# Kernel optimization log

Hardware: AMD Instinct MI355X
Metric: run time of the kernel (lower is better)

The kernel has to match this reference:

```python
import jax, jax.numpy as jnp
import numpy as np

N, D, F, C = 50000, 16, 128, 40  # nodes, fixed neighbor count, feat dim (hidden/2), classes


def _w(k, shape, fan_in):
    return jax.random.normal(k, shape, jnp.float32) / np.float32(np.sqrt(fan_in))


def setup_inputs() -> dict:
    key = jax.random.key(0)
    ks = jax.random.split(key, 8)
    z = lambda *s: jnp.zeros(s, jnp.float32)
    inp = {
        "x": jax.random.normal(ks[0], (N, F), jnp.float32),
        "edge_src": jax.random.randint(ks[1], (N, D), 0, N),  # dst is implicitly arange(N), sorted
        "W1": _w(ks[2], (F, F), F), "b1": z(F),
        "W2": _w(ks[3], (3 * F, F), F), "b2": z(3 * F),
        "W3": _w(ks[4], (F, 3 * F), 3 * F), "b3": z(F),
    }
    for i, (kb, oc) in (("1", (ks[5], F)), ("2", (ks[6], C))):
        pass  # placeholder (loop built below)
    for i, kb, oc in (("1", ks[5], F), ("2", ks[6], C)):
        kk = jax.random.split(kb, 5)
        inp["Wp" + i] = _w(kk[0], (F, F), F); inp["bp" + i] = z(F)
        inp["Wih" + i] = _w(kk[1], (4 * F, F), F)
        inp["Whh" + i] = _w(kk[2], (4 * F, F), F)
        inp["bih" + i] = z(4 * F); inp["bhh" + i] = z(4 * F)
        inp["Wl" + i] = _w(kk[3], (oc, F), F); inp["bl" + i] = z(oc)
        inp["Wr" + i] = _w(kk[4], (oc, F), F)
    return inp


def lstm_last(seq, Wih, Whh, bih, bhh):
    """seq: [N, T, F] -> final hidden state [N, H] (torch LSTM gate order i,f,g,o)."""
    Hh = Whh.shape[1]
    b = bih + bhh

    def step(carry, xt):
        h, c = carry
        g = xt @ Wih.T + h @ Whh.T + b
        i, f, gg, o = jnp.split(g, 4, axis=-1)
        c = jax.nn.sigmoid(f) * c + jax.nn.sigmoid(i) * jnp.tanh(gg)
        h = jax.nn.sigmoid(o) * jnp.tanh(c)
        return (h, c), None

    h0 = jnp.zeros((seq.shape[0], Hh), seq.dtype)
    (h, _), _ = jax.lax.scan(step, (h0, h0), jnp.swapaxes(seq, 0, 1))
    return h


def sage_conv_lstm(x, edge_src, Wp, bp, Wih, Whh, bih, bhh, Wl, bl, Wr):
    """PyG SAGEConv(aggr='lstm', project=True) with fixed per-node degree D."""
    xp = jax.nn.relu(x @ Wp.T + bp)           # project source features
    msgs = xp[edge_src]                        # [N, D, F] neighbor gather (sorted by dst)
    aggr = lstm_last(msgs, Wih, Whh, bih, bhh)  # LSTM over each neighborhood
    return aggr @ Wl.T + bl + x @ Wr.T         # lin_l(aggr) + lin_r(root)


def reference(x, edge_src, W1, b1, W2, b2, W3, b3,
              Wp1, bp1, Wih1, Whh1, bih1, bhh1, Wl1, bl1, Wr1,
              Wp2, bp2, Wih2, Whh2, bih2, bhh2, Wl2, bl2, Wr2):
    # Dead MLP branch: original forward computes it then overwrites h with conv1(x, ...)
    h = jax.nn.relu(x @ W1.T + b1)
    h = jax.nn.relu(h @ W2.T + b2)
    h = jax.nn.relu(h @ W3.T + b3)
    del h
    h = jax.nn.relu(sage_conv_lstm(x, edge_src, Wp1, bp1, Wih1, Whh1, bih1, bhh1, Wl1, bl1, Wr1))
    return sage_conv_lstm(h, edge_src, Wp2, bp2, Wih2, Whh2, bih2, bhh2, Wl2, bl2, Wr2)
```

## Files before the change

### kernel.cpp

```cpp
#include <hip/hip_runtime.h>
#include <hip/hip_bf16.h>


typedef __hip_bfloat16 bf16;
typedef __attribute__((ext_vector_type(8))) short short8;
typedef __attribute__((ext_vector_type(4))) short short4v;
typedef __attribute__((ext_vector_type(4))) float floatx4;

#define LOG2E 1.4426950408889634f
#define TWOL  2.8853900817779268f

__device__ __forceinline__ float bf2f(bf16 v) { return __bfloat162float(v); }
__device__ __forceinline__ bf16  f2bf(float v) { return __float2bfloat16(v); }
__device__ __forceinline__ float bfs2f(short s) {
    union { float f; unsigned u; } v; v.u = ((unsigned)(unsigned short)s) << 16; return v.f;
}
__device__ __forceinline__ short f2bfs(float v) {
    bf16 b = __float2bfloat16(v); return *(short*)&b;
}

__device__ __forceinline__ float ex2(float x) {
#if __has_builtin(__builtin_amdgcn_exp2f)
    return __builtin_amdgcn_exp2f(x);
#else
    return exp2f(x);
#endif
}

__device__ __forceinline__ float cell(float i_, float f_, float g_, float o_, float& c) {
    float ei = ex2(-i_), ef = ex2(-f_), eg = ex2(g_), eo = ex2(-o_);
    float A = (1.f + ei) * (eg + 1.f);
    float B = 1.f + ef;
    float cn = fmaf(c, A, fmaf(eg, TWOL, -TWOL) * B) * __builtin_amdgcn_rcpf(A * B);
    c = cn;
    float ec = ex2(cn);
    return (ec - 1.f) * __builtin_amdgcn_rcpf((ec + 1.f) * (1.f + eo));
}

__device__ __forceinline__ int ydecode(int p) {
    int pw = (p >> 6) & 7, pq = (p >> 4) & 3, pg = (p >> 2) & 3, pr = p & 3;
    return pg * 128 + pw * 16 + pq * 4 + pr;
}

__device__ __forceinline__ void dma2(const bf16* gp, void* lp0, void* lp1) {
    __builtin_amdgcn_global_load_lds(
        (const __attribute__((address_space(1))) void*)gp,
        (__attribute__((address_space(3))) void*)lp0, 16, 0, 0);
    __builtin_amdgcn_global_load_lds(
        (const __attribute__((address_space(1))) void*)(gp + 32),
        (__attribute__((address_space(3))) void*)lp1, 16, 0, 0);
}

struct Cvt { const void* src; bf16* dst; int n; int gs; };
struct CvtAll { Cvt t[19]; };

typedef __attribute__((ext_vector_type(4))) float float4v;

__global__ void convert_inputs(CvtAll ca, int* __restrict__ flag) {
    __shared__ int sflag;
    {
        const unsigned short* xb = (const unsigned short*)ca.t[0].src;
        int cnt = 0;
        for (int i = threadIdx.x; i < 1024; i += blockDim.x) {
            int e = (xb[i] >> 7) & 0xFF;
            cnt += (e >= 0xC8);
        }
        if (threadIdx.x == 0) sflag = 0;
        __syncthreads();
        if (cnt) atomicAdd(&sflag, cnt);
        __syncthreads();
    }
    const bool isf32 = (sflag >= 16);
    if (blockIdx.x == 0 && threadIdx.x == 0) *flag = isf32 ? 1 : 0;

    const int stride = gridDim.x * blockDim.x;
    const int tid0 = blockIdx.x * blockDim.x + threadIdx.x;
#pragma unroll 1
    for (int k = 0; k < 19; k++) {
        const int n = ca.t[k].n, gs = ca.t[k].gs;
        const int n8 = n >> 3;
        bf16* d = ca.t[k].dst;
        for (int i = tid0; i < n8; i += stride) {
            const int base = i << 3;
            float m = 1.f;
            if (gs) m = ((((unsigned)base >> gs) & 3) == 2) ? TWOL : LOG2E;
            short8 ov;
            if (isf32) {
                const float4v* sp = (const float4v*)ca.t[k].src;
                float4v a = sp[2 * i], b = sp[2 * i + 1];
#pragma unroll
                for (int j = 0; j < 4; j++) {
                    ov[j]     = f2bfs(a[j] * m);
                    ov[4 + j] = f2bfs(b[j] * m);
                }
            } else {
                short8 sv = ((const short8*)ca.t[k].src)[i];
                if (gs) {
#pragma unroll
                    for (int j = 0; j < 8; j++) ov[j] = f2bfs(bfs2f(sv[j]) * m);
                } else ov = sv;
            }
            ((short8*)d)[i] = ov;
        }
        for (int i = (n8 << 3) + tid0; i < n; i += stride) {
            float v = isf32 ? ((const float*)ca.t[k].src)[i]
                            : bfs2f(((const short*)ca.t[k].src)[i]);
            if (gs) v *= ((((unsigned)i >> gs) & 3) == 2) ? TWOL : LOG2E;
            d[i] = f2bf(v);
        }
    }
}

template <int NCT, bool RELU, bool BIAS2, bool DUAL, bool OUTF>
__global__ __launch_bounds__(256, 2) void gemm_bias(
    const bf16* __restrict__ A, const bf16* __restrict__ B,
    const bf16* __restrict__ bias, const bf16* __restrict__ bias2,
    const bf16* __restrict__ A2, const bf16* __restrict__ B2,
    void* __restrict__ Cv, const int* __restrict__ oflag,
    int N, int nbt, int ldc)
{
    const int tid = threadIdx.x;
    const int w = tid >> 6, l = tid & 63, q = l >> 4, lid = l & 15;
    const int rowbase = blockIdx.x * 64 + w * 16;
    const int colslice = blockIdx.y * (NCT * 16);

    int arow = rowbase + lid;
    if (arow >= N) arow = N - 1;

    floatx4 acc[NCT];
#pragma unroll
    for (int ct = 0; ct < NCT; ct++) acc[ct] = (floatx4)(0.f);

    short8 bfrag[NCT][4];
#pragma unroll
    for (int ct = 0; ct < NCT; ct++) {
        int j = colslice + ct * 16 + lid;
        if (j >= nbt) j = nbt - 1;
#pragma unroll
        for (int kt = 0; kt < 4; kt++)
            bfrag[ct][kt] = *(const short8*)(B + (size_t)j * 128 + kt * 32 + q * 8);
    }
#pragma unroll
    for (int kt = 0; kt < 4; kt++) {
        short8 af = *(const short8*)(A + (size_t)arow * 128 + kt * 32 + q * 8);
#pragma unroll
        for (int ct = 0; ct < NCT; ct++)
            acc[ct] = __builtin_amdgcn_mfma_f32_16x16x32_bf16(af, bfrag[ct][kt], acc[ct], 0, 0, 0);
    }
    if constexpr (DUAL) {
#pragma unroll
        for (int ct = 0; ct < NCT; ct++) {
            int j = colslice + ct * 16 + lid;
            if (j >= nbt) j = nbt - 1;
#pragma unroll
            for (int kt = 0; kt < 4; kt++)
                bfrag[ct][kt] = *(const short8*)(B2 + (size_t)j * 128 + kt * 32 + q * 8);
        }
#pragma unroll
        for (int kt = 0; kt < 4; kt++) {
            short8 af = *(const short8*)(A2 + (size_t)arow * 128 + kt * 32 + q * 8);
#pragma unroll
            for (int ct = 0; ct < NCT; ct++)
                acc[ct] = __builtin_amdgcn_mfma_f32_16x16x32_bf16(af, bfrag[ct][kt], acc[ct], 0, 0, 0);
        }
    }
    bool of32 = false;
    if constexpr (OUTF) of32 = (*oflag != 0);
#pragma unroll
    for (int ct = 0; ct < NCT; ct++) {
        int cg = colslice + ct * 16 + lid;
        int cb = cg < nbt ? cg : nbt - 1;
        float bv = bf2f(bias[cb]);
        if constexpr (BIAS2) bv += bf2f(bias2[cb]);
#pragma unroll
        for (int r = 0; r < 4; r++) {
            int row = rowbase + q * 4 + r;
            float v = acc[ct][r] + bv;
            if constexpr (RELU) v = fmaxf(v, 0.f);
            if (row < N && cg < nbt) {
                size_t idx = (size_t)row * ldc + cg;
                if constexpr (OUTF) {
                    if (of32) ((float*)Cv)[idx] = v;
                    else      ((bf16*)Cv)[idx] = f2bf(v);
                } else {
                    ((bf16*)Cv)[idx] = f2bf(v);
                }
            }
        }
    }
}

__global__ __launch_bounds__(256, 2) void fused_xp_y(
    const bf16* __restrict__ X, const bf16* __restrict__ Wp, const bf16* __restrict__ bp,
    const bf16* __restrict__ Wih, const bf16* __restrict__ bih, const bf16* __restrict__ bhh,
    bf16* __restrict__ Yout, int N)
{
    __shared__ bf16 T[64][136];
    const int tid = threadIdx.x;
    const int w = tid >> 6, l = tid & 63, q = l >> 4, lid = l & 15;
    const int rowbase = blockIdx.x * 64;

    int arow = rowbase + w * 16 + lid;
    if (arow >= N) arow = N - 1;

    floatx4 acc[8];
    short8 bfrag[8][4];
    float bvv[8];

#pragma unroll
    for (int ct = 0; ct < 8; ct++) acc[ct] = (floatx4)(0.f);
#pragma unroll
    for (int ct = 0; ct < 8; ct++) {
        int j = lid * 8 + ct;
        bvv[ct] = bf2f(bp[j]);
#pragma unroll
        for (int kt = 0; kt < 4; kt++)
            bfrag[ct][kt] = *(const short8*)(Wp + (size_t)j * 128 + kt * 32 + q * 8);
    }
#pragma unroll
    for (int kt = 0; kt < 4; kt++) {
        short8 af = *(const short8*)(X + (size_t)arow * 128 + kt * 32 + q * 8);
#pragma unroll
        for (int ct = 0; ct < 8; ct++)
            acc[ct] = __builtin_amdgcn_mfma_f32_16x16x32_bf16(af, bfrag[ct][kt], acc[ct], 0, 0, 0);
    }
#pragma unroll
    for (int r = 0; r < 4; r++) {
        short8 ov;
#pragma unroll
        for (int ct = 0; ct < 8; ct++)
            ov[ct] = f2bfs(fmaxf(acc[ct][r] + bvv[ct], 0.f));
        *(short8*)&T[w * 16 + q * 4 + r][lid * 8] = ov;
    }
    __syncthreads();

#pragma unroll 1
    for (int cc = 0; cc < 4; cc++) {
#pragma unroll
        for (int ct = 0; ct < 8; ct++) {
            int src = ydecode(cc * 128 + lid * 8 + ct);
            bvv[ct] = bf2f(bih[src]) + bf2f(bhh[src]);
#pragma unroll
            for (int kt = 0; kt < 4; kt++)
                bfrag[ct][kt] = *(const short8*)(Wih + (size_t)src * 128 + kt * 32 + q * 8);
        }
#pragma unroll
        for (int ct = 0; ct < 8; ct++) acc[ct] = (floatx4)(0.f);
#pragma unroll
        for (int kt = 0; kt < 4; kt++) {
            short8 af = *(const short8*)&T[w * 16 + lid][kt * 32 + q * 8];
#pragma unroll
            for (int ct = 0; ct < 8; ct++)
                acc[ct] = __builtin_amdgcn_mfma_f32_16x16x32_bf16(af, bfrag[ct][kt], acc[ct], 0, 0, 0);
        }
#pragma unroll
        for (int r = 0; r < 4; r++) {
            int row = rowbase + w * 16 + q * 4 + r;
            if (row < N) {
                short8 ov;
#pragma unroll
                for (int ct = 0; ct < 8; ct++)
                    ov[ct] = f2bfs(acc[ct][r] + bvv[ct]);
                *(short8*)(Yout + (size_t)row * 512 + cc * 128 + lid * 8) = ov;
            }
        }
    }
}

__global__ __launch_bounds__(256, 2) void fused_lin_xp_y(
    const bf16* __restrict__ aggr, const bf16* __restrict__ Wl, const bf16* __restrict__ bl,
    const bf16* __restrict__ X, const bf16* __restrict__ Wr,
    bf16* __restrict__ h1out,
    const bf16* __restrict__ Wp2, const bf16* __restrict__ bp2,
    const bf16* __restrict__ Wih2, const bf16* __restrict__ bih2, const bf16* __restrict__ bhh2,
    bf16* __restrict__ Yout, int N)
{
    __shared__ bf16 T1[64][136];
    __shared__ bf16 T2[64][136];
    const int tid = threadIdx.x;
    const int w = tid >> 6, l = tid & 63, q = l >> 4, lid = l & 15;
    const int rowbase = blockIdx.x * 64;

    int arow = rowbase + w * 16 + lid;
    if (arow >= N) arow = N - 1;

    floatx4 acc[8];
    short8 bfrag[8][4];
    float bvv[8];

#pragma unroll
    for (int ct = 0; ct < 8; ct++) acc[ct] = (floatx4)(0.f);
#pragma unroll
    for (int ct = 0; ct < 8; ct++) {
        int j = lid * 8 + ct;
        bvv[ct] = bf2f(bl[j]);
#pragma unroll
        for (int kt = 0; kt < 4; kt++)
            bfrag[ct][kt] = *(const short8*)(Wl + (size_t)j * 128 + kt * 32 + q * 8);
    }
#pragma unroll
    for (int kt = 0; kt < 4; kt++) {
        short8 af = *(const short8*)(aggr + (size_t)arow * 128 + kt * 32 + q * 8);
#pragma unroll
        for (int ct = 0; ct < 8; ct++)
            acc[ct] = __builtin_amdgcn_mfma_f32_16x16x32_bf16(af, bfrag[ct][kt], acc[ct], 0, 0, 0);
    }
#pragma unroll
    for (int ct = 0; ct < 8; ct++) {
        int j = lid * 8 + ct;
#pragma unroll
        for (int kt = 0; kt < 4; kt++)
            bfrag[ct][kt] = *(const short8*)(Wr + (size_t)j * 128 + kt * 32 + q * 8);
    }
#pragma unroll
    for (int kt = 0; kt < 4; kt++) {
        short8 af = *(const short8*)(X + (size_t)arow * 128 + kt * 32 + q * 8);
#pragma unroll
        for (int ct = 0; ct < 8; ct++)
            acc[ct] = __builtin_amdgcn_mfma_f32_16x16x32_bf16(af, bfrag[ct][kt], acc[ct], 0, 0, 0);
    }
#pragma unroll
    for (int r = 0; r < 4; r++) {
        short8 ov;
#pragma unroll
        for (int ct = 0; ct < 8; ct++)
            ov[ct] = f2bfs(fmaxf(acc[ct][r] + bvv[ct], 0.f));
        int rl = w * 16 + q * 4 + r;
        *(short8*)&T1[rl][lid * 8] = ov;
        int row = rowbase + rl;
        if (row < N) *(short8*)(h1out + (size_t)row * 128 + lid * 8) = ov;
    }
    __syncthreads();

#pragma unroll
    for (int ct = 0; ct < 8; ct++) {
        int j = lid * 8 + ct;
        bvv[ct] = bf2f(bp2[j]);
#pragma unroll
        for (int kt = 0; kt < 4; kt++)
            bfrag[ct][kt] = *(const short8*)(Wp2 + (size_t)j * 128 + kt * 32 + q * 8);
    }
#pragma unroll
    for (int ct = 0; ct < 8; ct++) acc[ct] = (floatx4)(0.f);
#pragma unroll
    for (int kt = 0; kt < 4; kt++) {
        short8 af = *(const short8*)&T1[w * 16 + lid][kt * 32 + q * 8];
#pragma unroll
        for (int ct = 0; ct < 8; ct++)
            acc[ct] = __builtin_amdgcn_mfma_f32_16x16x32_bf16(af, bfrag[ct][kt], acc[ct], 0, 0, 0);
    }
#pragma unroll
    for (int r = 0; r < 4; r++) {
        short8 ov;
#pragma unroll
        for (int ct = 0; ct < 8; ct++)
            ov[ct] = f2bfs(fmaxf(acc[ct][r] + bvv[ct], 0.f));
        *(short8*)&T2[w * 16 + q * 4 + r][lid * 8] = ov;
    }
    __syncthreads();

#pragma unroll 1
    for (int cc = 0; cc < 4; cc++) {
#pragma unroll
        for (int ct = 0; ct < 8; ct++) {
            int src = ydecode(cc * 128 + lid * 8 + ct);
            bvv[ct] = bf2f(bih2[src]) + bf2f(bhh2[src]);
#pragma unroll
            for (int kt = 0; kt < 4; kt++)
                bfrag[ct][kt] = *(const short8*)(Wih2 + (size_t)src * 128 + kt * 32 + q * 8);
        }
#pragma unroll
        for (int ct = 0; ct < 8; ct++) acc[ct] = (floatx4)(0.f);
#pragma unroll
        for (int kt = 0; kt < 4; kt++) {
            short8 af = *(const short8*)&T2[w * 16 + lid][kt * 32 + q * 8];
#pragma unroll
            for (int ct = 0; ct < 8; ct++)
                acc[ct] = __builtin_amdgcn_mfma_f32_16x16x32_bf16(af, bfrag[ct][kt], acc[ct], 0, 0, 0);
        }
#pragma unroll
        for (int r = 0; r < 4; r++) {
            int row = rowbase + w * 16 + q * 4 + r;
            if (row < N) {
                short8 ov;
#pragma unroll
                for (int ct = 0; ct < 8; ct++)
                    ov[ct] = f2bfs(acc[ct][r] + bvv[ct]);
                *(short8*)(Yout + (size_t)row * 512 + cc * 128 + lid * 8) = ov;
            }
        }
    }
}

__global__ __launch_bounds__(512, 4) void lstm_aggr(
    const bf16* __restrict__ Y,
    const int* __restrict__ esrc,
    const bf16* __restrict__ Whh,
    bf16* __restrict__ aggr,
    int N)
{
    __shared__ alignas(16) short stage[2][8][1024];
    __shared__ alignas(16) bf16 hb[2][16][136];
    __shared__ int srcl[16][16];

    const int tid = threadIdx.x;
    const int w = tid >> 6, l = tid & 63, q = l >> 4, lid = l & 15;
    const int nodebase = blockIdx.x * 16;

    if (tid < 256) {
        int node = tid >> 4, t = tid & 15;
        srcl[t][node] = esrc[(size_t)(nodebase + node) * 16 + t];
    }

    short8 wf[4][4];
#pragma unroll
    for (int g = 0; g < 4; g++) {
        int gc = g * 128 + 16 * w + lid;
#pragma unroll
        for (int kt = 0; kt < 4; kt++)
            wf[g][kt] = *(const short8*)(Whh + (size_t)gc * 128 + kt * 32 + q * 8);
    }

    float c[4];
#pragma unroll
    for (int r = 0; r < 4; r++) c[r] = 0.f;

    const int laneoff = w * 64 + q * 8;

    __syncthreads();

    {
        int s0 = srcl[0][lid];
        dma2(Y + (size_t)s0 * 512 + laneoff, &stage[0][w][0], &stage[0][w][512]);
        int s1 = srcl[1][lid];
        dma2(Y + (size_t)s1 * 512 + laneoff, &stage[1][w][0], &stage[1][w][512]);
    }

#pragma unroll 2
    for (int t = 0; t < 16; t++) {
        const int cb = t & 1;

        if (t == 15) asm volatile("s_waitcnt vmcnt(0)" ::: "memory");
        else         asm volatile("s_waitcnt vmcnt(2)" ::: "memory");

        int snext = (t < 14) ? srcl[t + 2][lid] : 0;

        floatx4 acc[4];
        {
            const short* wbuf = &stage[cb][w][0];
            short8 y0 = *(const short8*)&wbuf[q * 256 + lid * 8];
            short8 y1 = *(const short8*)&wbuf[q * 256 + 128 + lid * 8];
#pragma unroll
            for (int g = 0; g < 2; g++)
#pragma unroll
                for (int r = 0; r < 4; r++) {
                    acc[g][r]     = bfs2f(y0[g * 4 + r]);
                    acc[2 + g][r] = bfs2f(y1[g * 4 + r]);
                }
        }

        if (t) {
#pragma unroll
            for (int kt = 0; kt < 4; kt++) {
                short8 bh = *(const short8*)&hb[cb][lid][kt * 32 + q * 8];
#pragma unroll
                for (int g = 0; g < 4; g++)
                    acc[g] = __builtin_amdgcn_mfma_f32_16x16x32_bf16(wf[g][kt], bh, acc[g], 0, 0, 0);
            }
        }

        {
            short4v hv;
#pragma unroll
            for (int r = 0; r < 4; r++)
                hv[r] = f2bfs(cell(acc[0][r], acc[1][r], acc[2][r], acc[3][r], c[r]));
            if (t < 15) *(short4v*)&hb[cb ^ 1][lid][16 * w + 4 * q] = hv;
            else        *(short4v*)(aggr + (size_t)(nodebase + lid) * 128 + 16 * w + 4 * q) = hv;
        }

        if (t < 15) {
            asm volatile("s_waitcnt lgkmcnt(0)" ::: "memory");
            if (t < 14)
                dma2(Y + (size_t)snext * 512 + laneoff, &stage[cb][w][0], &stage[cb][w][512]);
            __builtin_amdgcn_s_barrier();
        }
    }
}

extern "C" void kernel_launch(void* const* d_in, const int* in_sizes, int n_in,
                              void* d_out, int out_size, void* d_ws, size_t ws_size,
                              hipStream_t stream)
{
    const int N = 50000;
    const int* es = (const int*)d_in[1];
    char* ws = (char*)d_ws;

    static const int idxs[19] = {0, 8,9,10,11,12,13,14,15,16, 17,18,19,20,21,22,23,24,25};
    static const int gss[19]  = {0, 0,0,14,14,7,7,0,0,0, 0,0,14,14,7,7,0,0,0};
    bf16* conv[19];
    size_t off = 0;
    CvtAll ca;
    for (int k = 0; k < 19; k++) {
        conv[k] = (bf16*)ws + off;
        ca.t[k].src = d_in[idxs[k]];
        ca.t[k].dst = conv[k];
        ca.t[k].n = in_sizes[idxs[k]];
        ca.t[k].gs = gss[k];
        off += (size_t)((in_sizes[idxs[k]] + 63) & ~63);
    }
    int* flag = (int*)(ws + ((size_t)15 << 20));
    bf16* aggr = (bf16*)(ws + ((size_t)16 << 20));
    bf16* Y    = (bf16*)(ws + ((size_t)30 << 20));
    bf16* h1   = (bf16*)(ws + ((size_t)84 << 20));

    const bf16 *xc  = conv[0];
    const bf16 *Wp1 = conv[1],  *bp1 = conv[2],  *Wih1 = conv[3],  *Whh1 = conv[4];
    const bf16 *bih1 = conv[5], *bhh1 = conv[6], *Wl1 = conv[7],   *bl1 = conv[8],  *Wr1 = conv[9];
    const bf16 *Wp2 = conv[10], *bp2 = conv[11], *Wih2 = conv[12], *Whh2 = conv[13];
    const bf16 *bih2 = conv[14], *bhh2 = conv[15], *Wl2 = conv[16], *bl2 = conv[17], *Wr2 = conv[18];

    dim3 blk(256);
    const int gx = (N + 63) / 64;
    const int gl = N / 16;

    convert_inputs<<<dim3(1024), blk, 0, stream>>>(ca, flag);

    fused_xp_y<<<dim3(gx), blk, 0, stream>>>(xc, Wp1, bp1, Wih1, bih1, bhh1, Y, N);
    lstm_aggr<<<dim3(gl), dim3(512), 0, stream>>>(Y, es, Whh1, aggr, N);

    fused_lin_xp_y<<<dim3(gx), blk, 0, stream>>>(
        aggr, Wl1, bl1, xc, Wr1, h1, Wp2, bp2, Wih2, bih2, bhh2, Y, N);
    lstm_aggr<<<dim3(gl), dim3(512), 0, stream>>>(Y, es, Whh2, aggr, N);

    gemm_bias<3, false, false, true, true><<<dim3(gx, 1), blk, 0, stream>>>(
        aggr, Wl2, bl2, nullptr, h1, Wr2, d_out, flag, N, 40, 40);
}
```

Measured before the change: 670.7 us.

## Fuse final linear layer into second LSTM kernel and pre-permute Wih weights

The final output GEMM (lin_l of aggr plus lin_r of h1) moves into the epilogue of the second LSTM aggregation kernel. The last hidden state stays in LDS and goes straight into MFMA, so one kernel launch and the aggr write/read round trip are gone. The conversion kernel also pre-permutes Wih rows into the ydecode order and precomputes the fp32 bias sum, which removes the index decode and double bias loads in the projection kernels. The cost is extra epilogue work and register pressure in the LSTM kernel, where only 3 of 8 waves do the tail GEMM.

```diff
diff --git a/kernel.cpp b/kernel.cpp
--- a/kernel.cpp
+++ b/kernel.cpp
@@ -6,6 +6,7 @@
 typedef __attribute__((ext_vector_type(8))) short short8;
 typedef __attribute__((ext_vector_type(4))) short short4v;
 typedef __attribute__((ext_vector_type(4))) float floatx4;
+typedef __attribute__((ext_vector_type(4))) float float4v;
 
 #define LOG2E 1.4426950408889634f
 #define TWOL  2.8853900817779268f
@@ -51,10 +52,8 @@
         (__attribute__((address_space(3))) void*)lp1, 16, 0, 0);
 }
 
-struct Cvt { const void* src; bf16* dst; int n; int gs; };
-struct CvtAll { Cvt t[19]; };
-
-typedef __attribute__((ext_vector_type(4))) float float4v;
+struct Cvt { const void* src; const void* src2; bf16* dst; int n; int mode; };
+struct CvtAll { Cvt t[17]; };
 
 __global__ void convert_inputs(CvtAll ca, int* __restrict__ flag) {
     __shared__ int sflag;
@@ -76,123 +75,66 @@
     const int stride = gridDim.x * blockDim.x;
     const int tid0 = blockIdx.x * blockDim.x + threadIdx.x;
 #pragma unroll 1
-    for (int k = 0; k < 19; k++) {
-        const int n = ca.t[k].n, gs = ca.t[k].gs;
+    for (int k = 0; k < 17; k++) {
+        const int n = ca.t[k].n, mode = ca.t[k].mode;
+        if (mode == 3) {
+            const float* a32 = (const float*)ca.t[k].src;
+            const float* b32 = (const float*)ca.t[k].src2;
+            const short* a16 = (const short*)ca.t[k].src;
+            const short* b16 = (const short*)ca.t[k].src2;
+            float* df = (float*)ca.t[k].dst;
+            for (int i = tid0; i < n; i += stride) {
+                int yd = ydecode(i);
+                float va = isf32 ? a32[yd] : bfs2f(a16[yd]);
+                float vb = isf32 ? b32[yd] : bfs2f(b16[yd]);
+                float m = ((((unsigned)i >> 2) & 3) == 2) ? TWOL : LOG2E;
+                df[i] = (va + vb) * m;
+            }
+            continue;
+        }
         const int n8 = n >> 3;
         bf16* d = ca.t[k].dst;
         for (int i = tid0; i < n8; i += stride) {
-            const int base = i << 3;
+            int si = i;
             float m = 1.f;
-            if (gs) m = ((((unsigned)base >> gs) & 3) == 2) ? TWOL : LOG2E;
+            bool scaled = false;
+            if (mode == 1) {
+                m = ((((unsigned)i >> 11) & 3) == 2) ? TWOL : LOG2E; scaled = true;
+            } else if (mode == 2) {
+                int row = i >> 4;
+                si = ydecode(row) * 16 + (i & 15);
+                m = ((((unsigned)row >> 2) & 3) == 2) ? TWOL : LOG2E; scaled = true;
+            }
             short8 ov;
             if (isf32) {
                 const float4v* sp = (const float4v*)ca.t[k].src;
-                float4v a = sp[2 * i], b = sp[2 * i + 1];
+                float4v a = sp[2 * si], b = sp[2 * si + 1];
 #pragma unroll
                 for (int j = 0; j < 4; j++) {
                     ov[j]     = f2bfs(a[j] * m);
                     ov[4 + j] = f2bfs(b[j] * m);
                 }
             } else {
-                short8 sv = ((const short8*)ca.t[k].src)[i];
-                if (gs) {
+                short8 sv = ((const short8*)ca.t[k].src)[si];
+                if (scaled) {
 #pragma unroll
                     for (int j = 0; j < 8; j++) ov[j] = f2bfs(bfs2f(sv[j]) * m);
                 } else ov = sv;
             }
             ((short8*)d)[i] = ov;
         }
-        for (int i = (n8 << 3) + tid0; i < n; i += stride) {
-            float v = isf32 ? ((const float*)ca.t[k].src)[i]
-                            : bfs2f(((const short*)ca.t[k].src)[i]);
-            if (gs) v *= ((((unsigned)i >> gs) & 3) == 2) ? TWOL : LOG2E;
-            d[i] = f2bf(v);
-        }
-    }
-}
-
-template <int NCT, bool RELU, bool BIAS2, bool DUAL, bool OUTF>
-__global__ __launch_bounds__(256, 2) void gemm_bias(
-    const bf16* __restrict__ A, const bf16* __restrict__ B,
-    const bf16* __restrict__ bias, const bf16* __restrict__ bias2,
-    const bf16* __restrict__ A2, const bf16* __restrict__ B2,
-    void* __restrict__ Cv, const int* __restrict__ oflag,
-    int N, int nbt, int ldc)
-{
-    const int tid = threadIdx.x;
-    const int w = tid >> 6, l = tid & 63, q = l >> 4, lid = l & 15;
-    const int rowbase = blockIdx.x * 64 + w * 16;
-    const int colslice = blockIdx.y * (NCT * 16);
-
-    int arow = rowbase + lid;
-    if (arow >= N) arow = N - 1;
-
-    floatx4 acc[NCT];
-#pragma unroll
-    for (int ct = 0; ct < NCT; ct++) acc[ct] = (floatx4)(0.f);
-
-    short8 bfrag[NCT][4];
-#pragma unroll
-    for (int ct = 0; ct < NCT; ct++) {
-        int j = colslice + ct * 16 + lid;
-        if (j >= nbt) j = nbt - 1;
-#pragma unroll
-        for (int kt = 0; kt < 4; kt++)
-            bfrag[ct][kt] = *(const short8*)(B + (size_t)j * 128 + kt * 32 + q * 8);
-    }
-#pragma unroll
-    for (int kt = 0; kt < 4; kt++) {
-        short8 af = *(const short8*)(A + (size_t)arow * 128 + kt * 32 + q * 8);
-#pragma unroll
-        for (int ct = 0; ct < NCT; ct++)
-            acc[ct] = __builtin_amdgcn_mfma_f32_16x16x32_bf16(af, bfrag[ct][kt], acc[ct], 0, 0, 0);
-    }
-    if constexpr (DUAL) {
-#pragma unroll
-        for (int ct = 0; ct < NCT; ct++) {
-            int j = colslice + ct * 16 + lid;
-            if (j >= nbt) j = nbt - 1;
-#pragma unroll
-            for (int kt = 0; kt < 4; kt++)
-                bfrag[ct][kt] = *(const short8*)(B2 + (size_t)j * 128 + kt * 32 + q * 8);
-        }
-#pragma unroll
-        for (int kt = 0; kt < 4; kt++) {
-            short8 af = *(const short8*)(A2 + (size_t)arow * 128 + kt * 32 + q * 8);
-#pragma unroll
-            for (int ct = 0; ct < NCT; ct++)
-                acc[ct] = __builtin_amdgcn_mfma_f32_16x16x32_bf16(af, bfrag[ct][kt], acc[ct], 0, 0, 0);
-        }
-    }
-    bool of32 = false;
-    if constexpr (OUTF) of32 = (*oflag != 0);
-#pragma unroll
-    for (int ct = 0; ct < NCT; ct++) {
-        int cg = colslice + ct * 16 + lid;
-        int cb = cg < nbt ? cg : nbt - 1;
-        float bv = bf2f(bias[cb]);
-        if constexpr (BIAS2) bv += bf2f(bias2[cb]);
-#pragma unroll
-        for (int r = 0; r < 4; r++) {
-            int row = rowbase + q * 4 + r;
-            float v = acc[ct][r] + bv;
-            if constexpr (RELU) v = fmaxf(v, 0.f);
-            if (row < N && cg < nbt) {
-                size_t idx = (size_t)row * ldc + cg;
-                if constexpr (OUTF) {
-                    if (of32) ((float*)Cv)[idx] = v;
-                    else      ((bf16*)Cv)[idx] = f2bf(v);
-                } else {
-                    ((bf16*)Cv)[idx] = f2bf(v);
-                }
-            }
-        }
+        if (mode == 0)
+            for (int i = (n8 << 3) + tid0; i < n; i += stride) {
+                float v = isf32 ? ((const float*)ca.t[k].src)[i]
+                                : bfs2f(((const short*)ca.t[k].src)[i]);
+                d[i] = f2bf(v);
+            }
     }
 }
 
 __global__ __launch_bounds__(256, 2) void fused_xp_y(
     const bf16* __restrict__ X, const bf16* __restrict__ Wp, const bf16* __restrict__ bp,
-    const bf16* __restrict__ Wih, const bf16* __restrict__ bih, const bf16* __restrict__ bhh,
+    const bf16* __restrict__ Wihp, const float* __restrict__ bsum,
     bf16* __restrict__ Yout, int N)
 {
     __shared__ bf16 T[64][136];
@@ -238,11 +180,11 @@
     for (int cc = 0; cc < 4; cc++) {
 #pragma unroll
         for (int ct = 0; ct < 8; ct++) {
-            int src = ydecode(cc * 128 + lid * 8 + ct);
-            bvv[ct] = bf2f(bih[src]) + bf2f(bhh[src]);
+            int pos = cc * 128 + lid * 8 + ct;
+            bvv[ct] = bsum[pos];
 #pragma unroll
             for (int kt = 0; kt < 4; kt++)
-                bfrag[ct][kt] = *(const short8*)(Wih + (size_t)src * 128 + kt * 32 + q * 8);
+                bfrag[ct][kt] = *(const short8*)(Wihp + (size_t)pos * 128 + kt * 32 + q * 8);
         }
 #pragma unroll
         for (int ct = 0; ct < 8; ct++) acc[ct] = (floatx4)(0.f);
@@ -272,7 +214,7 @@
     const bf16* __restrict__ X, const bf16* __restrict__ Wr,
     bf16* __restrict__ h1out,
     const bf16* __restrict__ Wp2, const bf16* __restrict__ bp2,
-    const bf16* __restrict__ Wih2, const bf16* __restrict__ bih2, const bf16* __restrict__ bhh2,
+    const bf16* __restrict__ Wihp2, const float* __restrict__ bsum2,
     bf16* __restrict__ Yout, int N)
 {
     __shared__ bf16 T1[64][136];
@@ -363,11 +305,11 @@
     for (int cc = 0; cc < 4; cc++) {
 #pragma unroll
         for (int ct = 0; ct < 8; ct++) {
-            int src = ydecode(cc * 128 + lid * 8 + ct);
-            bvv[ct] = bf2f(bih2[src]) + bf2f(bhh2[src]);
+            int pos = cc * 128 + lid * 8 + ct;
+            bvv[ct] = bsum2[pos];
 #pragma unroll
             for (int kt = 0; kt < 4; kt++)
-                bfrag[ct][kt] = *(const short8*)(Wih2 + (size_t)src * 128 + kt * 32 + q * 8);
+                bfrag[ct][kt] = *(const short8*)(Wihp2 + (size_t)pos * 128 + kt * 32 + q * 8);
         }
 #pragma unroll
         for (int ct = 0; ct < 8; ct++) acc[ct] = (floatx4)(0.f);
@@ -392,12 +334,16 @@
     }
 }
 
+template <int EPI>
 __global__ __launch_bounds__(512, 4) void lstm_aggr(
     const bf16* __restrict__ Y,
     const int* __restrict__ esrc,
     const bf16* __restrict__ Whh,
     bf16* __restrict__ aggr,
-    int N)
+    int N,
+    const bf16* __restrict__ Wl2, const bf16* __restrict__ bl2,
+    const bf16* __restrict__ Wr2, const bf16* __restrict__ h1,
+    void* __restrict__ outp, const int* __restrict__ oflag)
 {
     __shared__ alignas(16) short stage[2][8][1024];
     __shared__ alignas(16) bf16 hb[2][16][136];
@@ -475,7 +421,10 @@
             for (int r = 0; r < 4; r++)
                 hv[r] = f2bfs(cell(acc[0][r], acc[1][r], acc[2][r], acc[3][r], c[r]));
             if (t < 15) *(short4v*)&hb[cb ^ 1][lid][16 * w + 4 * q] = hv;
-            else        *(short4v*)(aggr + (size_t)(nodebase + lid) * 128 + 16 * w + 4 * q) = hv;
+            else if (EPI == 0)
+                *(short4v*)(aggr + (size_t)(nodebase + lid) * 128 + 16 * w + 4 * q) = hv;
+            else
+                *(short4v*)&hb[0][lid][16 * w + 4 * q] = hv;
         }
 
         if (t < 15) {
@@ -483,6 +432,44 @@
             if (t < 14)
                 dma2(Y + (size_t)snext * 512 + laneoff, &stage[cb][w][0], &stage[cb][w][512]);
             __builtin_amdgcn_s_barrier();
+        }
+    }
+
+    if constexpr (EPI == 1) {
+        asm volatile("s_waitcnt lgkmcnt(0)" ::: "memory");
+        __builtin_amdgcn_s_barrier();
+        if (w < 3) {
+            int j = w * 16 + lid;
+            int jc = j < 40 ? j : 39;
+            short8 blf[4], brf[4];
+#pragma unroll
+            for (int kt = 0; kt < 4; kt++) {
+                blf[kt] = *(const short8*)(Wl2 + (size_t)jc * 128 + kt * 32 + q * 8);
+                brf[kt] = *(const short8*)(Wr2 + (size_t)jc * 128 + kt * 32 + q * 8);
+            }
+            floatx4 o = (floatx4)(0.f);
+#pragma unroll
+            for (int kt = 0; kt < 4; kt++) {
+                short8 ah = *(const short8*)&hb[0][lid][kt * 32 + q * 8];
+                o = __builtin_amdgcn_mfma_f32_16x16x32_bf16(ah, blf[kt], o, 0, 0, 0);
+            }
+#pragma unroll
+            for (int kt = 0; kt < 4; kt++) {
+                short8 a1 = *(const short8*)(h1 + (size_t)(nodebase + lid) * 128 + kt * 32 + q * 8);
+                o = __builtin_amdgcn_mfma_f32_16x16x32_bf16(a1, brf[kt], o, 0, 0, 0);
+            }
+            float bv = bf2f(bl2[jc]);
+            bool of32 = (*oflag != 0);
+            if (j < 40) {
+#pragma unroll
+                for (int r = 0; r < 4; r++) {
+                    int node = nodebase + q * 4 + r;
+                    float v = o[r] + bv;
+                    size_t idx = (size_t)node * 40 + j;
+                    if (of32) ((float*)outp)[idx] = v;
+                    else      ((bf16*)outp)[idx]  = f2bf(v);
+                }
+            }
         }
     }
 }
@@ -495,29 +482,46 @@
     const int* es = (const int*)d_in[1];
     char* ws = (char*)d_ws;
 
-    static const int idxs[19] = {0, 8,9,10,11,12,13,14,15,16, 17,18,19,20,21,22,23,24,25};
-    static const int gss[19]  = {0, 0,0,14,14,7,7,0,0,0, 0,0,14,14,7,7,0,0,0};
-    bf16* conv[19];
+    struct Ent { int di; int di2; int mode; int n; };
+    Ent ents[17] = {
+        {0,  -1, 0, 0},
+        {8,  -1, 0, 0}, {9,  -1, 0, 0},
+        {10, -1, 2, 0}, {11, -1, 1, 0},
+        {12, 13, 3, 0},
+        {14, -1, 0, 0}, {15, -1, 0, 0}, {16, -1, 0, 0},
+        {17, -1, 0, 0}, {18, -1, 0, 0},
+        {19, -1, 2, 0}, {20, -1, 1, 0},
+        {21, 22, 3, 0},
+        {23, -1, 0, 0}, {24, -1, 0, 0}, {25, -1, 0, 0},
+    };
+    bf16* conv[17];
     size_t off = 0;
     CvtAll ca;
-    for (int k = 0; k < 19; k++) {
+    for (int k = 0; k < 17; k++) {
         conv[k] = (bf16*)ws + off;
-        ca.t[k].src = d_in[idxs[k]];
-        ca.t[k].dst = conv[k];
-        ca.t[k].n = in_sizes[idxs[k]];
-        ca.t[k].gs = gss[k];
-        off += (size_t)((in_sizes[idxs[k]] + 63) & ~63);
-    }
-    int* flag = (int*)(ws + ((size_t)15 << 20));
+        int n = in_sizes[ents[k].di];
+        ca.t[k].src  = d_in[ents[k].di];
+        ca.t[k].src2 = ents[k].di2 >= 0 ? d_in[ents[k].di2] : nullptr;
+        ca.t[k].dst  = conv[k];
+        ca.t[k].n    = n;
+        ca.t[k].mode = ents[k].mode;
+        size_t elems = (ents[k].mode == 3) ? (size_t)n * 2 : (size_t)n;
+        off += (elems + 63) & ~(size_t)63;
+    }
+    int* flag  = (int*)(ws + ((size_t)15 << 20));
     bf16* aggr = (bf16*)(ws + ((size_t)16 << 20));
     bf16* Y    = (bf16*)(ws + ((size_t)30 << 20));
     bf16* h1   = (bf16*)(ws + ((size_t)84 << 20));
 
-    const bf16 *xc  = conv[0];
-    const bf16 *Wp1 = conv[1],  *bp1 = conv[2],  *Wih1 = conv[3],  *Whh1 = conv[4];
-    const bf16 *bih1 = conv[5], *bhh1 = conv[6], *Wl1 = conv[7],   *bl1 = conv[8],  *Wr1 = conv[9];
-    const bf16 *Wp2 = conv[10], *bp2 = conv[11], *Wih2 = conv[12], *Whh2 = conv[13];
-    const bf16 *bih2 = conv[14], *bhh2 = conv[15], *Wl2 = conv[16], *bl2 = conv[17], *Wr2 = conv[18];
+    const bf16 *xc   = conv[0];
+    const bf16 *Wp1  = conv[1],  *bp1 = conv[2];
+    const bf16 *Wihp1 = conv[3], *Whh1 = conv[4];
+    const float *bsum1 = (const float*)conv[5];
+    const bf16 *Wl1 = conv[6], *bl1 = conv[7], *Wr1 = conv[8];
+    const bf16 *Wp2 = conv[9], *bp2 = conv[10];
+    const bf16 *Wihp2 = conv[11], *Whh2 = conv[12];
+    const float *bsum2 = (const float*)conv[13];
+    const bf16 *Wl2 = conv[14], *bl2 = conv[15], *Wr2 = conv[16];
 
     dim3 blk(256);
     const int gx = (N + 63) / 64;
@@ -525,13 +529,13 @@
 
     convert_inputs<<<dim3(1024), blk, 0, stream>>>(ca, flag);
 
-    fused_xp_y<<<dim3(gx), blk, 0, stream>>>(xc, Wp1, bp1, Wih1, bih1, bhh1, Y, N);
-    lstm_aggr<<<dim3(gl), dim3(512), 0, stream>>>(Y, es, Whh1, aggr, N);
+    fused_xp_y<<<dim3(gx), blk, 0, stream>>>(xc, Wp1, bp1, Wihp1, bsum1, Y, N);
+    lstm_aggr<0><<<dim3(gl), dim3(512), 0, stream>>>(
+        Y, es, Whh1, aggr, N, nullptr, nullptr, nullptr, nullptr, nullptr, nullptr);
 
     fused_lin_xp_y<<<dim3(gx), blk, 0, stream>>>(
-        aggr, Wl1, bl1, xc, Wr1, h1, Wp2, bp2, Wih2, bih2, bhh2, Y, N);
-    lstm_aggr<<<dim3(gl), dim3(512), 0, stream>>>(Y, es, Whh2, aggr, N);
-
-    gemm_bias<3, false, false, true, true><<<dim3(gx, 1), blk, 0, stream>>>(
-        aggr, Wl2, bl2, nullptr, h1, Wr2, d_out, flag, N, 40, 40);
-}
+        aggr, Wl1, bl1, xc, Wr1, h1, Wp2, bp2, Wihp2, bsum2, Y, N);
+
+    lstm_aggr<1><<<dim3(gl), dim3(512), 0, stream>>>(
+        Y, es, Whh2, aggr, N, Wl2, bl2, Wr2, h1, d_out, flag);
+}
```

Result: faster. 655.5 us (-2.3%).
